# Performance work log

Hardware: AMD Instinct MI355X
Metric: run time of the kernel (lower is better)

## Reference

```python
import jax, jax.numpy as jnp
import numpy as np

B, T, D, H, MLP, NI, OUT = 256, 2049, 64, 64, 128, 128, 10
L = D + D * (D - 1) // 2  # depth-2 logsignature channels = 2080


def _logsig_depth2(X, n_intervals):
    """Depth-2 log-signature of a piecewise-linear path over equal intervals.
    X: [B, T, D] with T = n_intervals*s + 1. Returns [B, n_intervals, L] where
    L = D + D(D-1)/2 (level-1 increments + strictly-upper-triangular Levy areas,
    the Lyndon-word basis signatory uses at depth 2)."""
    Bq, Tq, Dq = X.shape
    s = (Tq - 1) // n_intervals
    idx = np.arange(n_intervals)[:, None] * s + np.arange(s + 1)[None, :]
    seg = X[:, idx]                       # [B, n, s+1, D]
    inc = seg[:, :, -1] - seg[:, :, 0]    # level 1: [B, n, D]
    dlt = seg[:, :, 1:] - seg[:, :, :-1]  # per-step increments [B, n, s, D]
    cum = seg[:, :, :-1] - seg[:, :, :1]  # partial increments  [B, n, s, D]
    M = jnp.einsum('bnki,bnkj->bnij', cum, dlt)
    A = 0.5 * (M - jnp.swapaxes(M, -1, -2))  # Levy area [B, n, D, D]
    iu, ju = np.triu_indices(Dq, 1)
    return jnp.concatenate([inc, A[..., iu, ju]], axis=-1)  # [B, n, L]


def setup_inputs() -> dict:
    key = jax.random.key(0)
    ks = jax.random.split(key, 10)
    X = jax.random.normal(ks[0], (B, T, D), jnp.float32) * 0.05
    W_in = jax.random.normal(ks[1], (D, H), jnp.float32) / np.sqrt(D)
    b_in = jnp.zeros((H,), jnp.float32)
    W1 = jax.random.normal(ks[2], (H, MLP), jnp.float32) / np.sqrt(H)
    b1 = jnp.zeros((MLP,), jnp.float32)
    W2 = jax.random.normal(ks[3], (MLP, D * L), jnp.float32) / np.sqrt(MLP)
    b2 = jnp.zeros((D * L,), jnp.float32)
    W_out = jax.random.normal(ks[4], (H, OUT), jnp.float32) / np.sqrt(H)
    b_out = jnp.zeros((OUT,), jnp.float32)
    return {"X": X, "W_in": W_in, "b_in": b_in, "W1": W1, "b1": b1,
            "W2": W2, "b2": b2, "W_out": W_out, "b_out": b_out,
            "n_intervals": NI}


def reference(X, W_in, b_in, W1, b1, W2, b2, W_out, b_out, n_intervals):
    Bq, Tq, Dq = X.shape
    logsig = _logsig_depth2(X, n_intervals)        # [B, n, L]
    h0 = X[:, 0] @ W_in + b_in                     # initial_linear

    def vf(h):  # F.forward: MLP(h) -> [B, D, L]
        z = jnp.tanh(h @ W1 + b1)
        return (z @ W2 + b2).reshape(Bq, Dq, -1)

    def g(h, ls):  # f(h) contracted with logsig derivative
        return jnp.einsum('bdl,bl->bd', vf(h), ls)

    def rk4_step(h, ls):  # one RK4 step per interval, dt = 1
        k1 = g(h, ls)
        k2 = g(h + 0.5 * k1, ls)
        k3 = g(h + 0.5 * k2, ls)
        k4 = g(h + k3, ls)
        return h + (k1 + 2.0 * k2 + 2.0 * k3 + k4) / 6.0, None

    hT, _ = jax.lax.scan(rk4_step, h0, jnp.swapaxes(logsig, 0, 1))
    return hT @ W_out + b_out  # readout_linear: [B, OUT]
```

## Files before the change

kernel.cpp:

```cpp
#include <hip/hip_runtime.h>
#include <hip/hip_bf16.h>
#include <cstdint>
#include <cstddef>

#define B_SZ   256
#define T_SZ   2049
#define D_SZ   64
#define H_SZ   64
#define MLP_SZ 128
#define NI_SZ  128
#define SEG    16
#define KDIM   2080
#define KP     2112
#define OUT_SZ 10

#define NC     32
#define NCHUNK (NI_SZ / NC)
#define MROWS  (NC * B_SZ)
#define NB     8448
#define GSTR   8256
#define NT     (KP / 64)

typedef _Float16 f16x8 __attribute__((ext_vector_type(8)));
typedef float    f32x4 __attribute__((ext_vector_type(4)));

__device__ __forceinline__ float rlane(float v, int l) {
    return __uint_as_float(__builtin_amdgcn_readlane(__float_as_uint(v), l));
}

__global__ __launch_bounds__(256) void build_B(const float* __restrict__ W2,
                                               const float* __restrict__ b2,
                                               _Float16* __restrict__ Bm) {
    const int r = blockIdx.x, t = threadIdx.x;
    const float* src = nullptr;
    if (r < 8192) {
        const int d = r >> 7, m = r & 127;
        src = W2 + (size_t)m * (64 * KDIM) + (size_t)d * KDIM;
    } else if (r < 8256) {
        src = b2 + (size_t)(r - 8192) * KDIM;
    }
    _Float16* dst = Bm + (size_t)r * KP;
    for (int l = t; l < KP; l += 256)
        dst[l] = (src && l < KDIM) ? (_Float16)src[l] : (_Float16)0.0f;
}

__global__ void h0_kernel(const float* __restrict__ X, const float* __restrict__ W_in,
                          const float* __restrict__ b_in, float* __restrict__ h_state) {
    const int b = blockIdx.x, t = threadIdx.x;
    __shared__ float x0[D_SZ];
    if (t < D_SZ) x0[t] = X[(size_t)b * T_SZ * D_SZ + t];
    __syncthreads();
    float acc = b_in[t];
    for (int k = 0; k < D_SZ; ++k) acc += x0[k] * W_in[k * H_SZ + t];
    h_state[b * H_SZ + t] = acc;
}

__global__ __launch_bounds__(256) void logsig_kernel(const float* __restrict__ X,
                                                     _Float16* __restrict__ LS,
                                                     int n0) {
    const int b = blockIdx.x, sl = blockIdx.y, t = threadIdx.x;
    const int n = n0 + sl;
    __shared__ float seg[SEG + 1][D_SZ];
    __shared__ float cum[SEG][D_SZ];
    __shared__ float dlt[SEG][D_SZ];
    __shared__ float Mm[D_SZ][D_SZ + 1];

    const float* Xp = X + ((size_t)b * T_SZ + (size_t)n * SEG) * D_SZ;
    for (int i = t; i < (SEG + 1) * D_SZ / 4; i += 256)
        ((float4*)&seg[0][0])[i] = ((const float4*)Xp)[i];
    __syncthreads();
    for (int i = t; i < SEG * D_SZ; i += 256) {
        const int k = i >> 6, d = i & 63;
        cum[k][d] = seg[k][d] - seg[0][d];
        dlt[k][d] = seg[k + 1][d] - seg[k][d];
    }
    __syncthreads();

    const int ti = t >> 4, tj = t & 15;
    const int i0 = ti * 4, j0 = tj * 4;
    float m4[4][4] = {};
#pragma unroll
    for (int k = 0; k < SEG; ++k) {
        const float4 ci = *(const float4*)&cum[k][i0];
        const float4 dj = *(const float4*)&dlt[k][j0];
        const float* cip = (const float*)&ci;
        const float* djp = (const float*)&dj;
#pragma unroll
        for (int a = 0; a < 4; ++a)
#pragma unroll
            for (int c = 0; c < 4; ++c)
                m4[a][c] += cip[a] * djp[c];
    }
#pragma unroll
    for (int a = 0; a < 4; ++a)
#pragma unroll
        for (int c = 0; c < 4; ++c)
            Mm[i0 + a][j0 + c] = m4[a][c];
    __syncthreads();

    _Float16* out = LS + (size_t)(sl * B_SZ + b) * KP;
    if (t < D_SZ) out[t] = (_Float16)(seg[SEG][t] - seg[0][t]);
    if (t < KP - KDIM) out[KDIM + t] = (_Float16)0.0f;
    if (tj >= ti) {
#pragma unroll
        for (int a = 0; a < 4; ++a) {
            const int i = i0 + a;
#pragma unroll
            for (int c = 0; c < 4; ++c) {
                const int j = j0 + c;
                if (j > i) {
                    const int p = 63 * i - (i * (i - 1)) / 2 + (j - i - 1);
                    out[D_SZ + p] = (_Float16)(0.5f * (m4[a][c] - Mm[j][i]));
                }
            }
        }
    }
}

#define GLDS(SRC, DST) __builtin_amdgcn_global_load_lds(                        \
    (__attribute__((address_space(1))) void*)(SRC),                             \
    (__attribute__((address_space(3))) void*)(DST), 16, 0, 0)

#define STAGE(KT, KK, BUF) do {                                                 \
    const unsigned short* _sa = Asrc + (size_t)(KT) * 64 + (KK) * 32;           \
    const unsigned short* _sb = Bsrc + (size_t)(KT) * 64 + (KK) * 32;           \
    unsigned short* _d = ldst + (BUF) * 32768 + (KK) * 8192;                    \
    GLDS(_sa,                  _d);                                             \
    GLDS(_sa + (size_t)128*KP, _d + 4096);                                      \
    GLDS(_sb,                  _d + 16384);                                     \
    GLDS(_sb + (size_t)128*KP, _d + 20480);                                     \
} while (0)

#define BAR() do { __builtin_amdgcn_s_barrier(); __builtin_amdgcn_sched_barrier(0); } while (0)

#define VMW_(N) asm volatile("s_waitcnt vmcnt(" #N ")" ::: "memory")
#define VMW(N) VMW_(N)

#define LOAD_A(KK, MB) do {                                                     \
    af0 = *(const f16x8*)(aC + (KK) * 8192 + ((MB) + 0) * 512);                 \
    af1 = *(const f16x8*)(aC + (KK) * 8192 + ((MB) + 1) * 512);                 \
    af2 = *(const f16x8*)(aC + (KK) * 8192 + ((MB) + 2) * 512);                 \
    af3 = *(const f16x8*)(aC + (KK) * 8192 + ((MB) + 3) * 512);                 \
} while (0)

#define LOAD_B(KK) do {                                                         \
    bg0 = *(const f16x8*)(bC + (KK) * 8192 + 0 * 512);                          \
    bg1 = *(const f16x8*)(bC + (KK) * 8192 + 1 * 512);                          \
    bg2 = *(const f16x8*)(bC + (KK) * 8192 + 2 * 512);                          \
    bg3 = *(const f16x8*)(bC + (KK) * 8192 + 3 * 512);                          \
} while (0)

#define MFMA16(MB) do {                                                         \
    __builtin_amdgcn_s_setprio(1);                                              \
    acc[(MB)+0][0] = __builtin_amdgcn_mfma_f32_16x16x32_f16(af0, bg0, acc[(MB)+0][0], 0, 0, 0); \
    acc[(MB)+0][1] = __builtin_amdgcn_mfma_f32_16x16x32_f16(af0, bg1, acc[(MB)+0][1], 0, 0, 0); \
    acc[(MB)+1][0] = __builtin_amdgcn_mfma_f32_16x16x32_f16(af1, bg0, acc[(MB)+1][0], 0, 0, 0); \
    acc[(MB)+1][1] = __builtin_amdgcn_mfma_f32_16x16x32_f16(af1, bg1, acc[(MB)+1][1], 0, 0, 0); \
    acc[(MB)+0][2] = __builtin_amdgcn_mfma_f32_16x16x32_f16(af0, bg2, acc[(MB)+0][2], 0, 0, 0); \
    acc[(MB)+0][3] = __builtin_amdgcn_mfma_f32_16x16x32_f16(af0, bg3, acc[(MB)+0][3], 0, 0, 0); \
    acc[(MB)+1][2] = __builtin_amdgcn_mfma_f32_16x16x32_f16(af1, bg2, acc[(MB)+1][2], 0, 0, 0); \
    acc[(MB)+1][3] = __builtin_amdgcn_mfma_f32_16x16x32_f16(af1, bg3, acc[(MB)+1][3], 0, 0, 0); \
    acc[(MB)+2][0] = __builtin_amdgcn_mfma_f32_16x16x32_f16(af2, bg0, acc[(MB)+2][0], 0, 0, 0); \
    acc[(MB)+2][1] = __builtin_amdgcn_mfma_f32_16x16x32_f16(af2, bg1, acc[(MB)+2][1], 0, 0, 0); \
    acc[(MB)+3][0] = __builtin_amdgcn_mfma_f32_16x16x32_f16(af3, bg0, acc[(MB)+3][0], 0, 0, 0); \
    acc[(MB)+3][1] = __builtin_amdgcn_mfma_f32_16x16x32_f16(af3, bg1, acc[(MB)+3][1], 0, 0, 0); \
    acc[(MB)+2][2] = __builtin_amdgcn_mfma_f32_16x16x32_f16(af2, bg2, acc[(MB)+2][2], 0, 0, 0); \
    acc[(MB)+2][3] = __builtin_amdgcn_mfma_f32_16x16x32_f16(af2, bg3, acc[(MB)+2][3], 0, 0, 0); \
    acc[(MB)+3][2] = __builtin_amdgcn_mfma_f32_16x16x32_f16(af3, bg2, acc[(MB)+3][2], 0, 0, 0); \
    acc[(MB)+3][3] = __builtin_amdgcn_mfma_f32_16x16x32_f16(af3, bg3, acc[(MB)+3][3], 0, 0, 0); \
    __builtin_amdgcn_s_setprio(0);                                              \
} while (0)

#define TILE_BODY(TT, CUR, DOS1, DOS0, V1, V2) do {                             \
    const unsigned short* aC = aP + (CUR) * 32768;                              \
    const unsigned short* bC = bP + (CUR) * 32768;                              \
                                  \
    if (DOS1) { STAGE((TT) + 1, 1, (CUR) ^ 1); }                                \
    LOAD_B(0); LOAD_A(0, 0);                                                    \
    BAR(); MFMA16(0); BAR();                                                    \
                                                                        \
    LOAD_A(0, 4);                                                               \
    BAR(); MFMA16(4); VMW(V1); BAR();                                           \
                                    \
    if (DOS0) { STAGE((TT) + 2, 0, (CUR)); }                                    \
    LOAD_B(1); LOAD_A(1, 0);                                                    \
    BAR(); MFMA16(0); BAR();                                                    \
                                                                        \
    LOAD_A(1, 4);                                                               \
    BAR(); MFMA16(4); VMW(V2); BAR();                                           \
} while (0)

__global__ __launch_bounds__(512, 2) void gemm256(const unsigned short* __restrict__ A,
                                                  const unsigned short* __restrict__ Bm,
                                                  _Float16* __restrict__ C) {
    __shared__ __align__(16) unsigned short lds[65536];
    const int t = threadIdx.x;

    const int wg = blockIdx.x;
    int bx, by0, nit;
    if (wg < 32) {
        bx = (wg & 7) * 4 + (wg >> 3);
        by0 = bx;
        nit = 2;
    } else {
        const int idx = (wg - 32) >> 3;
        bx = (wg & 7) * 4 + idx / 31;
        const int byi = idx % 31;
        by0 = byi + (byi >= bx ? 1 : 0);
        nit = 1;
    }
    const int tileM = bx * 256;

    const int q7s = (t >> 3) & 7;
    const int u   = (t & 7) ^ q7s;
    const int strow = ((t >> 3) << 1) + (u >> 2);
    const int stcol = (u & 3) << 3;
    const unsigned short* Asrc = A + (size_t)(tileM + strow) * KP + stcol;
    unsigned short* ldst = lds + t * 8;

    const int lane = t & 63, w = t >> 6;
    const int wm = w >> 2, wn = w & 3;
    const int frow = lane & 15, j4 = lane >> 4;
    const int fr2 = frow >> 1;
    const int slot = (((frow & 1) << 2) | j4) ^ fr2;
    const unsigned short* aP = lds + wm * 4096 + fr2 * 64 + slot * 8;
    const unsigned short* bP = lds + 16384 + wn * 2048 + fr2 * 64 + slot * 8;

#pragma unroll 1
    for (int it = 0; it < nit; ++it) {
        const int tileN = (it == 0 ? by0 : 32) * 256;
        const unsigned short* Bsrc = Bm + (size_t)(tileN + strow) * KP + stcol;

        f32x4 acc[8][4] = {};
        f16x8 af0, af1, af2, af3, bg0, bg1, bg2, bg3;

        STAGE(0, 0, 0);
        STAGE(0, 1, 0);
        STAGE(1, 0, 1);
        VMW(8);
        BAR();

        int cur = 0;
#pragma unroll 1
        for (int tt = 0; tt < NT - 2; ++tt) {
            TILE_BODY(tt, cur, 1, 1, 8, 8);
            cur ^= 1;
        }
        TILE_BODY(NT - 2, cur, 1, 0, 8, 4);
        cur ^= 1;
        TILE_BODY(NT - 1, cur, 0, 0, 0, 0);

        const int erow = j4 << 2;
#pragma unroll
        for (int mi = 0; mi < 8; ++mi) {
            const int grow = tileM + wm * 128 + mi * 16 + erow;
#pragma unroll
            for (int ni = 0; ni < 4; ++ni) {
                const int gcol = tileN + wn * 64 + ni * 16 + frow;
                if (gcol < GSTR) {
                    _Float16* cp = C + (size_t)grow * GSTR + gcol;
#pragma unroll
                    for (int r = 0; r < 4; ++r)
                        cp[(size_t)r * GSTR] = (_Float16)acc[mi][ni][r];
                }
            }
        }
    }
}

__global__ __launch_bounds__(256) void ode_chunk(const _Float16* __restrict__ G,
                                                 const float* __restrict__ W1,
                                                 const float* __restrict__ b1,
                                                 float* __restrict__ h_state) {
    const int b = blockIdx.x, t = threadIdx.x;
    const int lane = t & 63, w = t >> 6;
    const int j0 = w * 32 + (lane & 31);
    __shared__ float ysw[4][D_SZ];
    __shared__ float part[2][4][D_SZ];

    float w1c[D_SZ];
#pragma unroll
    for (int dd = 0; dd < D_SZ; ++dd) w1c[dd] = W1[dd * MLP_SZ + j0];
    const float b1v = b1[j0];

    float hsv = h_state[b * H_SZ + lane];
    ysw[w][lane] = hsv;
    float k_st[4] = {0.f, 0.f, 0.f, 0.f};

    f16x8 pr[4];
    _Float16 b2pre;
    {
        const _Float16* Gr = G + (size_t)b * GSTR;
        const f16x8* gp = (const f16x8*)(Gr + lane * 128 + w * 32);
#pragma unroll
        for (int v = 0; v < 4; ++v) pr[v] = gp[v];
        b2pre = Gr[8192 + lane];
    }

#pragma unroll 1
    for (int s = 0; s < NC; ++s) {
        float gcur[32];
#pragma unroll
        for (int v = 0; v < 4; ++v)
#pragma unroll
            for (int e = 0; e < 8; ++e) gcur[v * 8 + e] = (float)pr[v][e];
        const float b2cur = (float)b2pre;
        if (s + 1 < NC) {
            const _Float16* Gr = G + (size_t)((s + 1) * B_SZ + b) * GSTR;
            const f16x8* gp = (const f16x8*)(Gr + lane * 128 + w * 32);
#pragma unroll
            for (int v = 0; v < 4; ++v) pr[v] = gp[v];
            b2pre = Gr[8192 + lane];
        }

#pragma unroll
        for (int st = 0; st < 4; ++st) {
            float ax = 0.f, ay = 0.f, az = 0.f, aw = 0.f;
#pragma unroll
            for (int dd = 0; dd < D_SZ; dd += 4) {
                const float4 yv = *(const float4*)&ysw[w][dd];
                ax += yv.x * w1c[dd];
                ay += yv.y * w1c[dd + 1];
                az += yv.z * w1c[dd + 2];
                aw += yv.w * w1c[dd + 3];
            }
            const float xx = b1v + ((ax + ay) + (az + aw));
            const float ex = __expf(2.0f * xx);
            const float z = 1.0f - 2.0f / (ex + 1.0f);
            float s0 = 0.f, s1 = 0.f, s2 = 0.f, s3 = 0.f;
#pragma unroll
            for (int q = 0; q < 32; q += 4) {
                s0 += gcur[q]     * rlane(z, q);
                s1 += gcur[q + 1] * rlane(z, q + 1);
                s2 += gcur[q + 2] * rlane(z, q + 2);
                s3 += gcur[q + 3] * rlane(z, q + 3);
            }
            part[st & 1][w][lane] = (s0 + s1) + (s2 + s3);
            __syncthreads();
            const float kv = b2cur + part[st & 1][0][lane] + part[st & 1][1][lane]
                           + part[st & 1][2][lane] + part[st & 1][3][lane];
            k_st[st] = kv;
            if (st < 3) {
                float y = hsv;
                if (st == 0) y += 0.5f * kv;
                else if (st == 1) y += 0.5f * kv;
                else y += kv;
                ysw[w][lane] = y;
            }
        }
        hsv += (k_st[0] + 2.0f * k_st[1] + 2.0f * k_st[2] + k_st[3]) * (1.0f / 6.0f);
        ysw[w][lane] = hsv;
    }
    if (w == 0) h_state[b * H_SZ + lane] = hsv;
}

__global__ void out_kernel(const float* __restrict__ h_state, const float* __restrict__ W_out,
                           const float* __restrict__ b_out, float* __restrict__ out) {
    const int b = blockIdx.x, t = threadIdx.x;
    __shared__ float hh[H_SZ];
    hh[t] = h_state[b * H_SZ + t];
    __syncthreads();
    if (t < OUT_SZ) {
        float acc = b_out[t];
        for (int d = 0; d < H_SZ; ++d) acc += hh[d] * W_out[d * OUT_SZ + t];
        out[b * OUT_SZ + t] = acc;
    }
}

extern "C" void kernel_launch(void* const* d_in, const int* in_sizes, int n_in,
                              void* d_out, int out_size, void* d_ws, size_t ws_size,
                              hipStream_t stream) {
    (void)in_sizes; (void)n_in; (void)out_size; (void)ws_size;
    const float* X     = (const float*)d_in[0];
    const float* W_in  = (const float*)d_in[1];
    const float* b_in  = (const float*)d_in[2];
    const float* W1    = (const float*)d_in[3];
    const float* b1    = (const float*)d_in[4];
    const float* W2    = (const float*)d_in[5];
    const float* b2    = (const float*)d_in[6];
    const float* W_out = (const float*)d_in[7];
    const float* b_out = (const float*)d_in[8];
    float* out = (float*)d_out;

    char* ws = (char*)d_ws;
    size_t off = 0;
    auto take = [&](size_t bytes) { void* p = ws + off; off = (off + bytes + 255) & ~(size_t)255; return p; };
    _Float16* Bmat = (_Float16*)take((size_t)NB * KP * 2);
    _Float16* LSc  = (_Float16*)take((size_t)MROWS * KP * 2);
    _Float16* G    = (_Float16*)take((size_t)MROWS * GSTR * 2);
    float*    hst  = (float*)take((size_t)B_SZ * H_SZ * 4);

    build_B<<<NB, 256, 0, stream>>>(W2, b2, Bmat);
    h0_kernel<<<B_SZ, H_SZ, 0, stream>>>(X, W_in, b_in, hst);

    for (int c = 0; c < NCHUNK; ++c) {
        logsig_kernel<<<dim3(B_SZ, NC), 256, 0, stream>>>(X, LSc, c * NC);
        gemm256<<<dim3(1024), 512, 0, stream>>>(
            (const unsigned short*)LSc, (const unsigned short*)Bmat, G);
        ode_chunk<<<B_SZ, 256, 0, stream>>>(G, W1, b1, hst);
    }
    out_kernel<<<B_SZ, H_SZ, 0, stream>>>(hst, W_out, b_out, out);
}
```

Measured before the change: 2.072 ms.

## Double-buffer LDS fragment registers in GEMM and simplify tile assignment

The GEMM inner loop now keeps two sets of A/B fragment registers, so LDS reads for the next MFMA group are issued before the current MFMA group runs. This removes the barrier that sat between each fragment load and its MFMAs, and it prefetches the first fragments of the next K tile. The launch grows from 1024 to 1056 workgroups, one 256x256 tile each, replacing the old scheme where 32 workgroups computed two tiles. The costs are higher register pressure, looser vmcnt waits that must still order correctly against the global-to-LDS copies, and an uneven last wave of workgroups.

```diff
diff --git a/kernel.cpp b/kernel.cpp
--- a/kernel.cpp
+++ b/kernel.cpp
@@ -131,63 +131,74 @@
     GLDS(_sb + (size_t)128*KP, _d + 20480);                                     \
 } while (0)
 
-#define BAR() do { __builtin_amdgcn_s_barrier(); __builtin_amdgcn_sched_barrier(0); } while (0)
+#define BAR() do {                                                              \
+    __builtin_amdgcn_sched_barrier(0);                                          \
+    __builtin_amdgcn_s_barrier();                                               \
+    __builtin_amdgcn_sched_barrier(0);                                          \
+} while (0)
 
 #define VMW_(N) asm volatile("s_waitcnt vmcnt(" #N ")" ::: "memory")
 #define VMW(N) VMW_(N)
 
-#define LOAD_A(KK, MB) do {                                                     \
-    af0 = *(const f16x8*)(aC + (KK) * 8192 + ((MB) + 0) * 512);                 \
-    af1 = *(const f16x8*)(aC + (KK) * 8192 + ((MB) + 1) * 512);                 \
-    af2 = *(const f16x8*)(aC + (KK) * 8192 + ((MB) + 2) * 512);                 \
-    af3 = *(const f16x8*)(aC + (KK) * 8192 + ((MB) + 3) * 512);                 \
-} while (0)
-
-#define LOAD_B(KK) do {                                                         \
-    bg0 = *(const f16x8*)(bC + (KK) * 8192 + 0 * 512);                          \
-    bg1 = *(const f16x8*)(bC + (KK) * 8192 + 1 * 512);                          \
-    bg2 = *(const f16x8*)(bC + (KK) * 8192 + 2 * 512);                          \
-    bg3 = *(const f16x8*)(bC + (KK) * 8192 + 3 * 512);                          \
-} while (0)
-
-#define MFMA16(MB) do {                                                         \
+#define RD_A(S, PTR, KK, MB) do {                                               \
+    a##S##0 = *(const f16x8*)((PTR) + (KK) * 8192 + ((MB) + 0) * 512);          \
+    a##S##1 = *(const f16x8*)((PTR) + (KK) * 8192 + ((MB) + 1) * 512);          \
+    a##S##2 = *(const f16x8*)((PTR) + (KK) * 8192 + ((MB) + 2) * 512);          \
+    a##S##3 = *(const f16x8*)((PTR) + (KK) * 8192 + ((MB) + 3) * 512);          \
+} while (0)
+
+#define RD_B(S, PTR, KK) do {                                                   \
+    b##S##0 = *(const f16x8*)((PTR) + (KK) * 8192 + 0 * 512);                   \
+    b##S##1 = *(const f16x8*)((PTR) + (KK) * 8192 + 1 * 512);                   \
+    b##S##2 = *(const f16x8*)((PTR) + (KK) * 8192 + 2 * 512);                   \
+    b##S##3 = *(const f16x8*)((PTR) + (KK) * 8192 + 3 * 512);                   \
+} while (0)
+
+#define MFMA16(MB, AS, BS) do {                                                 \
     __builtin_amdgcn_s_setprio(1);                                              \
-    acc[(MB)+0][0] = __builtin_amdgcn_mfma_f32_16x16x32_f16(af0, bg0, acc[(MB)+0][0], 0, 0, 0); \
-    acc[(MB)+0][1] = __builtin_amdgcn_mfma_f32_16x16x32_f16(af0, bg1, acc[(MB)+0][1], 0, 0, 0); \
-    acc[(MB)+1][0] = __builtin_amdgcn_mfma_f32_16x16x32_f16(af1, bg0, acc[(MB)+1][0], 0, 0, 0); \
-    acc[(MB)+1][1] = __builtin_amdgcn_mfma_f32_16x16x32_f16(af1, bg1, acc[(MB)+1][1], 0, 0, 0); \
-    acc[(MB)+0][2] = __builtin_amdgcn_mfma_f32_16x16x32_f16(af0, bg2, acc[(MB)+0][2], 0, 0, 0); \
-    acc[(MB)+0][3] = __builtin_amdgcn_mfma_f32_16x16x32_f16(af0, bg3, acc[(MB)+0][3], 0, 0, 0); \
-    acc[(MB)+1][2] = __builtin_amdgcn_mfma_f32_16x16x32_f16(af1, bg2, acc[(MB)+1][2], 0, 0, 0); \
-    acc[(MB)+1][3] = __builtin_amdgcn_mfma_f32_16x16x32_f16(af1, bg3, acc[(MB)+1][3], 0, 0, 0); \
-    acc[(MB)+2][0] = __builtin_amdgcn_mfma_f32_16x16x32_f16(af2, bg0, acc[(MB)+2][0], 0, 0, 0); \
-    acc[(MB)+2][1] = __builtin_amdgcn_mfma_f32_16x16x32_f16(af2, bg1, acc[(MB)+2][1], 0, 0, 0); \
-    acc[(MB)+3][0] = __builtin_amdgcn_mfma_f32_16x16x32_f16(af3, bg0, acc[(MB)+3][0], 0, 0, 0); \
-    acc[(MB)+3][1] = __builtin_amdgcn_mfma_f32_16x16x32_f16(af3, bg1, acc[(MB)+3][1], 0, 0, 0); \
-    acc[(MB)+2][2] = __builtin_amdgcn_mfma_f32_16x16x32_f16(af2, bg2, acc[(MB)+2][2], 0, 0, 0); \
-    acc[(MB)+2][3] = __builtin_amdgcn_mfma_f32_16x16x32_f16(af2, bg3, acc[(MB)+2][3], 0, 0, 0); \
-    acc[(MB)+3][2] = __builtin_amdgcn_mfma_f32_16x16x32_f16(af3, bg2, acc[(MB)+3][2], 0, 0, 0); \
-    acc[(MB)+3][3] = __builtin_amdgcn_mfma_f32_16x16x32_f16(af3, bg3, acc[(MB)+3][3], 0, 0, 0); \
+    acc[(MB)+0][0] = __builtin_amdgcn_mfma_f32_16x16x32_f16(a##AS##0, b##BS##0, acc[(MB)+0][0], 0, 0, 0); \
+    acc[(MB)+0][1] = __builtin_amdgcn_mfma_f32_16x16x32_f16(a##AS##0, b##BS##1, acc[(MB)+0][1], 0, 0, 0); \
+    acc[(MB)+1][0] = __builtin_amdgcn_mfma_f32_16x16x32_f16(a##AS##1, b##BS##0, acc[(MB)+1][0], 0, 0, 0); \
+    acc[(MB)+1][1] = __builtin_amdgcn_mfma_f32_16x16x32_f16(a##AS##1, b##BS##1, acc[(MB)+1][1], 0, 0, 0); \
+    acc[(MB)+0][2] = __builtin_amdgcn_mfma_f32_16x16x32_f16(a##AS##0, b##BS##2, acc[(MB)+0][2], 0, 0, 0); \
+    acc[(MB)+0][3] = __builtin_amdgcn_mfma_f32_16x16x32_f16(a##AS##0, b##BS##3, acc[(MB)+0][3], 0, 0, 0); \
+    acc[(MB)+1][2] = __builtin_amdgcn_mfma_f32_16x16x32_f16(a##AS##1, b##BS##2, acc[(MB)+1][2], 0, 0, 0); \
+    acc[(MB)+1][3] = __builtin_amdgcn_mfma_f32_16x16x32_f16(a##AS##1, b##BS##3, acc[(MB)+1][3], 0, 0, 0); \
+    acc[(MB)+2][0] = __builtin_amdgcn_mfma_f32_16x16x32_f16(a##AS##2, b##BS##0, acc[(MB)+2][0], 0, 0, 0); \
+    acc[(MB)+2][1] = __builtin_amdgcn_mfma_f32_16x16x32_f16(a##AS##2, b##BS##1, acc[(MB)+2][1], 0, 0, 0); \
+    acc[(MB)+3][0] = __builtin_amdgcn_mfma_f32_16x16x32_f16(a##AS##3, b##BS##0, acc[(MB)+3][0], 0, 0, 0); \
+    acc[(MB)+3][1] = __builtin_amdgcn_mfma_f32_16x16x32_f16(a##AS##3, b##BS##1, acc[(MB)+3][1], 0, 0, 0); \
+    acc[(MB)+2][2] = __builtin_amdgcn_mfma_f32_16x16x32_f16(a##AS##2, b##BS##2, acc[(MB)+2][2], 0, 0, 0); \
+    acc[(MB)+2][3] = __builtin_amdgcn_mfma_f32_16x16x32_f16(a##AS##2, b##BS##3, acc[(MB)+2][3], 0, 0, 0); \
+    acc[(MB)+3][2] = __builtin_amdgcn_mfma_f32_16x16x32_f16(a##AS##3, b##BS##2, acc[(MB)+3][2], 0, 0, 0); \
+    acc[(MB)+3][3] = __builtin_amdgcn_mfma_f32_16x16x32_f16(a##AS##3, b##BS##3, acc[(MB)+3][3], 0, 0, 0); \
     __builtin_amdgcn_s_setprio(0);                                              \
 } while (0)
 
-#define TILE_BODY(TT, CUR, DOS1, DOS0, V1, V2) do {                             \
+#define TILE_BODY(TT, CUR, DOS1, DOS0, RDN, V1, V2) do {                        \
     const unsigned short* aC = aP + (CUR) * 32768;                              \
     const unsigned short* bC = bP + (CUR) * 32768;                              \
-                                  \
+    const unsigned short* aN = aP + ((CUR) ^ 1) * 32768;                        \
+    const unsigned short* bN = bP + ((CUR) ^ 1) * 32768;                        \
+                                                                        \
     if (DOS1) { STAGE((TT) + 1, 1, (CUR) ^ 1); }                                \
-    LOAD_B(0); LOAD_A(0, 0);                                                    \
-    BAR(); MFMA16(0); BAR();                                                    \
+    RD_A(1, aC, 0, 4);                                                          \
+    MFMA16(0, 0, 0);                                                            \
+    BAR();                                                                      \
                                                                         \
-    LOAD_A(0, 4);                                                               \
-    BAR(); MFMA16(4); VMW(V1); BAR();                                           \
-                                    \
+    RD_A(0, aC, 1, 0);                                                          \
+    RD_B(1, bC, 1);                                                             \
+    MFMA16(4, 1, 0);                                                            \
+    VMW(V1); BAR();                                                             \
+                                                                        \
     if (DOS0) { STAGE((TT) + 2, 0, (CUR)); }                                    \
-    LOAD_B(1); LOAD_A(1, 0);                                                    \
-    BAR(); MFMA16(0); BAR();                                                    \
+    RD_A(1, aC, 1, 4);                                                          \
+    MFMA16(0, 0, 1);                                                            \
+    BAR();                                                                      \
                                                                         \
-    LOAD_A(1, 4);                                                               \
-    BAR(); MFMA16(4); VMW(V2); BAR();                                           \
+    if (RDN) { RD_A(0, aN, 0, 0); RD_B(0, bN, 0); }                             \
+    MFMA16(4, 1, 1);                                                            \
+    VMW(V2); BAR();                                                             \
 } while (0)
 
 __global__ __launch_bounds__(512, 2) void gemm256(const unsigned short* __restrict__ A,
@@ -197,25 +208,16 @@
     const int t = threadIdx.x;
 
     const int wg = blockIdx.x;
-    int bx, by0, nit;
-    if (wg < 32) {
-        bx = (wg & 7) * 4 + (wg >> 3);
-        by0 = bx;
-        nit = 2;
-    } else {
-        const int idx = (wg - 32) >> 3;
-        bx = (wg & 7) * 4 + idx / 31;
-        const int byi = idx % 31;
-        by0 = byi + (byi >= bx ? 1 : 0);
-        nit = 1;
-    }
-    const int tileM = bx * 256;
+    const int x  = (wg & 7) * 132 + (wg >> 3);
+    const int bx = x / 33, by = x % 33;
+    const int tileM = bx * 256, tileN = by * 256;
 
     const int q7s = (t >> 3) & 7;
     const int u   = (t & 7) ^ q7s;
     const int strow = ((t >> 3) << 1) + (u >> 2);
     const int stcol = (u & 3) << 3;
-    const unsigned short* Asrc = A + (size_t)(tileM + strow) * KP + stcol;
+    const unsigned short* Asrc = A  + (size_t)(tileM + strow) * KP + stcol;
+    const unsigned short* Bsrc = Bm + (size_t)(tileN + strow) * KP + stcol;
     unsigned short* ldst = lds + t * 8;
 
     const int lane = t & 63, w = t >> 6;
@@ -226,43 +228,40 @@
     const unsigned short* aP = lds + wm * 4096 + fr2 * 64 + slot * 8;
     const unsigned short* bP = lds + 16384 + wn * 2048 + fr2 * 64 + slot * 8;
 
+    f32x4 acc[8][4] = {};
+    f16x8 a00, a01, a02, a03, a10, a11, a12, a13;
+    f16x8 b00, b01, b02, b03, b10, b11, b12, b13;
+
+    STAGE(0, 0, 0);
+    STAGE(0, 1, 0);
+    STAGE(1, 0, 1);
+    VMW(4);
+    BAR();
+    RD_A(0, aP, 0, 0);
+    RD_B(0, bP, 0);
+
+    int cur = 0;
 #pragma unroll 1
-    for (int it = 0; it < nit; ++it) {
-        const int tileN = (it == 0 ? by0 : 32) * 256;
-        const unsigned short* Bsrc = Bm + (size_t)(tileN + strow) * KP + stcol;
-
-        f32x4 acc[8][4] = {};
-        f16x8 af0, af1, af2, af3, bg0, bg1, bg2, bg3;
-
-        STAGE(0, 0, 0);
-        STAGE(0, 1, 0);
-        STAGE(1, 0, 1);
-        VMW(8);
-        BAR();
-
-        int cur = 0;
-#pragma unroll 1
-        for (int tt = 0; tt < NT - 2; ++tt) {
-            TILE_BODY(tt, cur, 1, 1, 8, 8);
-            cur ^= 1;
-        }
-        TILE_BODY(NT - 2, cur, 1, 0, 8, 4);
+    for (int tt = 0; tt < NT - 2; ++tt) {
+        TILE_BODY(tt, cur, 1, 1, 1, 4, 4);
         cur ^= 1;
-        TILE_BODY(NT - 1, cur, 0, 0, 0, 0);
-
-        const int erow = j4 << 2;
-#pragma unroll
-        for (int mi = 0; mi < 8; ++mi) {
-            const int grow = tileM + wm * 128 + mi * 16 + erow;
-#pragma unroll
-            for (int ni = 0; ni < 4; ++ni) {
-                const int gcol = tileN + wn * 64 + ni * 16 + frow;
-                if (gcol < GSTR) {
-                    _Float16* cp = C + (size_t)grow * GSTR + gcol;
-#pragma unroll
-                    for (int r = 0; r < 4; ++r)
-                        cp[(size_t)r * GSTR] = (_Float16)acc[mi][ni][r];
-                }
+    }
+    TILE_BODY(NT - 2, cur, 1, 0, 1, 4, 0);
+    cur ^= 1;
+    TILE_BODY(NT - 1, cur, 0, 0, 0, 0, 0);
+
+    const int erow = j4 << 2;
+#pragma unroll
+    for (int mi = 0; mi < 8; ++mi) {
+        const int grow = tileM + wm * 128 + mi * 16 + erow;
+#pragma unroll
+        for (int ni = 0; ni < 4; ++ni) {
+            const int gcol = tileN + wn * 64 + ni * 16 + frow;
+            if (gcol < GSTR) {
+                _Float16* cp = C + (size_t)grow * GSTR + gcol;
+#pragma unroll
+                for (int r = 0; r < 4; ++r)
+                    cp[(size_t)r * GSTR] = (_Float16)acc[mi][ni][r];
             }
         }
     }
@@ -395,7 +394,7 @@
 
     for (int c = 0; c < NCHUNK; ++c) {
         logsig_kernel<<<dim3(B_SZ, NC), 256, 0, stream>>>(X, LSc, c * NC);
-        gemm256<<<dim3(1024), 512, 0, stream>>>(
+        gemm256<<<dim3(1056), 512, 0, stream>>>(
             (const unsigned short*)LSc, (const unsigned short*)Bmat, G);
         ode_chunk<<<B_SZ, 256, 0, stream>>>(G, W1, b1, hst);
     }
```

New measurement: 1.975 ms. 1.05x faster.
